# Kernel tuning notes

Hardware: AMD Instinct MI355X
Metric: run time of the kernel (lower is better)

The kernel has to match this reference:

```python
import jax, jax.numpy as jnp
import numpy as np

SEP_ID = 102  # bert-base [SEP]


def setup_inputs() -> dict:
    key = jax.random.key(0)
    B, S, H, M = 64, 512, 768, 21
    k1, k2, k3, k4 = jax.random.split(key, 4)
    hidden = jax.random.normal(k1, (B, S, H), dtype=jnp.float32)  # tf1 last_hidden_state
    ids = jax.random.randint(k2, (B, S), 1000, 30000)
    sep_pos = jnp.arange(24, 24 * (M + 1), 24)  # 21 sep positions < 512
    ids = ids.at[:, sep_pos].set(SEP_ID)
    W = jax.random.normal(k3, (H, H), dtype=jnp.float32) * 0.02  # nn.Linear weight [out,in]
    b = jnp.zeros((H,), dtype=jnp.float32)
    v = jax.random.normal(k4, (H,), dtype=jnp.float32) * 0.02    # linear_value [H,1] squeezed
    return {"hidden": hidden, "input_ids": ids, "W": W, "b": b, "v": v,
            "max_sent_count": M}


def _segment_attention_pool(hidden, input_ids, W, b, v, M):
    B, S, H = hidden.shape
    sep = input_ids == SEP_ID                                 # [B,S] bool
    csum = jnp.cumsum(sep.astype(jnp.int32), axis=1)
    seg = csum - sep.astype(jnp.int32)                        # seps strictly before t
    nsep = csum[:, -1]                                        # sentences per row
    pos = jnp.arange(S)
    # sentence k = tokens strictly between sep k-1 and sep k, excluding CLS (pos 0)
    valid = (~sep) & (pos[None, :] >= 1) & (seg < nsep[:, None]) & (seg < M)

    # attention scores: tanh(x @ W.T + b) @ v
    scores = jnp.einsum('bsh,h->bs', jnp.tanh(jnp.einsum('bsh,kh->bsk', hidden, W) + b), v)

    NS = B * M + 1                                            # +1 dummy segment for invalid tokens
    fid = jnp.where(valid, jnp.arange(B)[:, None] * M + seg, B * M).reshape(-1)
    sflat = jnp.where(valid, scores, -jnp.inf).reshape(-1)

    # per-segment stable softmax
    m = jax.ops.segment_max(sflat, fid, num_segments=NS)
    m = jnp.where(jnp.isfinite(m), m, 0.0)                    # empty segments
    e = jnp.where(valid.reshape(-1), jnp.exp(sflat - m[fid]), 0.0)
    denom = jax.ops.segment_sum(e, fid, num_segments=NS)
    w = e / jnp.where(denom[fid] > 0, denom[fid], 1.0)

    sent = jax.ops.segment_sum(w[:, None] * hidden.reshape(-1, H), fid,
                               num_segments=NS)[:B * M].reshape(B, M, H)
    # rows with zero sentences fall back to the CLS embedding (original behavior)
    sent = sent.at[:, 0, :].set(jnp.where((nsep == 0)[:, None], hidden[:, 0, :], sent[:, 0, :]))
    return sent


def reference(hidden, input_ids, W, b, v, max_sent_count):
    return _segment_attention_pool(hidden, input_ids, W, b, v, max_sent_count)
```

## Files before the change

### kernel.cpp

```cpp
#include <hip/hip_runtime.h>


#define SEP_ID 102
#define Bn 64
#define Sn 512
#define Hn 768
#define Mn 21
#define BS (Bn * Sn)

typedef __attribute__((ext_vector_type(8))) short bf16x8;
typedef __attribute__((ext_vector_type(8))) unsigned short u16x8;
typedef __attribute__((ext_vector_type(4))) float f32x4;

__device__ inline unsigned short f2bf(float x) {
  unsigned int u = __builtin_bit_cast(unsigned int, x);
  u += 0x7fffu + ((u >> 16) & 1u);
  return (unsigned short)(u >> 16);
}

__device__ inline u16x8 cvt8v(f32x4 a, f32x4 b) {
  u16x8 r;
  r[0] = f2bf(a[0]); r[1] = f2bf(a[1]); r[2] = f2bf(a[2]); r[3] = f2bf(a[3]);
  r[4] = f2bf(b[0]); r[5] = f2bf(b[1]); r[6] = f2bf(b[2]); r[7] = f2bf(b[3]);
  return r;
}

__device__ inline float tanh_fast(float x) {
  float e = __builtin_amdgcn_exp2f(x * 2.885390081777927f);
  return 1.f - 2.f * __builtin_amdgcn_rcpf(e + 1.f);
}

__global__ void convw_kernel(const float* __restrict__ W, unsigned short* __restrict__ WBp) {
  int c = blockIdx.x * 256 + threadIdx.x;
  int nt = c / 1536;
  int r  = c % 1536;
  int ks = r >> 6;
  int ln = r & 63;
  int col = nt * 16 + (ln & 15);
  int k0  = ks * 32 + (ln >> 4) * 8;
  const f32x4* src = reinterpret_cast<const f32x4*>(&W[col * Hn + k0]);
  f32x4 a = src[0];
  f32x4 b = src[1];
  *reinterpret_cast<u16x8*>(&WBp[(size_t)c * 8]) = cvt8v(a, b);
}

__global__ void segscan_kernel(const int* __restrict__ ids,
                               unsigned char* __restrict__ segv,
                               int* __restrict__ nsep) {
  int b = blockIdx.x;
  int s = threadIdx.x;
  __shared__ int cs[Sn];
  int sep = (ids[b * Sn + s] == SEP_ID) ? 1 : 0;
  cs[s] = sep;
  __syncthreads();
  for (int off = 1; off < Sn; off <<= 1) {
    int add = (s >= off) ? cs[s - off] : 0;
    __syncthreads();
    cs[s] += add;
    __syncthreads();
  }
  int csum = cs[s];
  int nb = cs[Sn - 1];
  int seg = csum - sep;
  bool valid = (!sep) && (s >= 1) && (seg < nb) && (seg < Mn);
  segv[b * Sn + s] = valid ? (unsigned char)seg : (unsigned char)0xFF;
  if (s == 0) nsep[b] = nb;
}

__global__ __launch_bounds__(1024, 4) void score_gemm_kernel(
    const float* __restrict__ hid, const unsigned short* __restrict__ WBp,
    const float* __restrict__ bbias, const float* __restrict__ vvec,
    float* __restrict__ scores) {
  __shared__ __align__(16) unsigned short As[64 * 768];
  __shared__ float scpart[16][64];

  const int t = threadIdx.x;
  const size_t rowBase = (size_t)blockIdx.x * 64;
  const int wid = t >> 6, lane = t & 63;
  const int l15 = lane & 15, l4 = lane >> 4;
  const int colBase = wid * 48;

  {
    const int srow = t >> 4;
    const int scloc = t & 15;
    const f32x4* hsrc = reinterpret_cast<const f32x4*>(
        &hid[(rowBase + srow) * Hn + scloc * 8]);
    unsigned short* const arow = &As[srow * Hn];
    const int swz = srow & 7;
    f32x4 p[6][2];
#pragma unroll
    for (int cc = 0; cc < 6; ++cc) {
      p[cc][0] = __builtin_nontemporal_load(hsrc + cc * 32);
      p[cc][1] = __builtin_nontemporal_load(hsrc + cc * 32 + 1);
    }
#pragma unroll
    for (int cc = 0; cc < 6; ++cc)
      *reinterpret_cast<u16x8*>(arow + ((cc * 16 + scloc) ^ swz) * 8) =
          cvt8v(p[cc][0], p[cc][1]);
  }
  __syncthreads();

  const unsigned short* const afrow = &As[l15 * Hn];
  const int aswz = l15 & 7;
  const unsigned short* bp0 = &WBp[((size_t)(wid * 3 + 0) * 24 * 64 + lane) * 8];
  const unsigned short* bp1 = &WBp[((size_t)(wid * 3 + 1) * 24 * 64 + lane) * 8];
  const unsigned short* bp2 = &WBp[((size_t)(wid * 3 + 2) * 24 * 64 + lane) * 8];

  f32x4 acc[4][3];
#pragma unroll
  for (int mi = 0; mi < 4; ++mi)
#pragma unroll
    for (int ni = 0; ni < 3; ++ni) acc[mi][ni] = (f32x4){0.f, 0.f, 0.f, 0.f};

  bf16x8 br[4][3];
#pragma unroll
  for (int s = 0; s < 3; ++s) {
    br[s][0] = *reinterpret_cast<const bf16x8*>(bp0 + s * 512);
    br[s][1] = *reinterpret_cast<const bf16x8*>(bp1 + s * 512);
    br[s][2] = *reinterpret_cast<const bf16x8*>(bp2 + s * 512);
  }

#pragma unroll
  for (int kk = 0; kk < 24; ++kk) {
    bf16x8 af[4];
#pragma unroll
    for (int mi = 0; mi < 4; ++mi)
      af[mi] = *reinterpret_cast<const bf16x8*>(
          &afrow[mi * 16 * Hn + (((kk * 4 + l4) ^ aswz)) * 8]);
    if (kk + 3 < 24) {
      const int sl = (kk + 3) & 3;
      br[sl][0] = *reinterpret_cast<const bf16x8*>(bp0 + (kk + 3) * 512);
      br[sl][1] = *reinterpret_cast<const bf16x8*>(bp1 + (kk + 3) * 512);
      br[sl][2] = *reinterpret_cast<const bf16x8*>(bp2 + (kk + 3) * 512);
    }
    const int cu = kk & 3;
    __builtin_amdgcn_s_setprio(1);
#pragma unroll
    for (int mi = 0; mi < 4; ++mi)
#pragma unroll
      for (int ni = 0; ni < 3; ++ni)
        acc[mi][ni] = __builtin_amdgcn_mfma_f32_16x16x32_bf16(
            af[mi], br[cu][ni], acc[mi][ni], 0, 0, 0);
    __builtin_amdgcn_s_setprio(0);
  }

  float sc[4][4];
#pragma unroll
  for (int mi = 0; mi < 4; ++mi)
#pragma unroll
    for (int r = 0; r < 4; ++r) sc[mi][r] = 0.f;
#pragma unroll
  for (int ni = 0; ni < 3; ++ni) {
    int col = colBase + ni * 16 + l15;
    float vv = vvec[col];
    float bb = bbias[col];
#pragma unroll
    for (int mi = 0; mi < 4; ++mi)
#pragma unroll
      for (int r = 0; r < 4; ++r)
        sc[mi][r] += tanh_fast(acc[mi][ni][r] + bb) * vv;
  }
#pragma unroll
  for (int off = 1; off < 16; off <<= 1)
#pragma unroll
    for (int mi = 0; mi < 4; ++mi)
#pragma unroll
      for (int r = 0; r < 4; ++r)
        sc[mi][r] += __shfl_xor(sc[mi][r], off, 64);
  if (l15 == 0) {
#pragma unroll
    for (int mi = 0; mi < 4; ++mi)
#pragma unroll
      for (int r = 0; r < 4; ++r)
        scpart[wid][mi * 16 + l4 * 4 + r] = sc[mi][r];
  }
  __syncthreads();
  if (t < 64) {
    float s = 0.f;
#pragma unroll
    for (int w = 0; w < 16; ++w) s += scpart[w][t];
    scores[rowBase + t] = s;
  }
}

__global__ __launch_bounds__(256) void pool_kernel(
    const float* __restrict__ hid, const float* __restrict__ scores,
    const unsigned char* __restrict__ segv, const int* __restrict__ nsep,
    float* __restrict__ out) {
  int bm = blockIdx.x;
  int b = bm / Mn, m = bm % Mn;
  int t = threadIdx.x;
  __shared__ float wLds[Sn];
  __shared__ float red[256];
  __shared__ int ired[256];
  const float NEG = -1e30f;

  int base = b * Sn;
  unsigned char mg = (unsigned char)m;
  unsigned char g0 = segv[base + t], g1 = segv[base + 256 + t];
  bool v0 = (g0 == mg), v1 = (g1 == mg);
  float s0 = v0 ? scores[base + t] : NEG;
  float s1 = v1 ? scores[base + 256 + t] : NEG;

  red[t] = fmaxf(s0, s1);
  __syncthreads();
  for (int o = 128; o > 0; o >>= 1) {
    if (t < o) red[t] = fmaxf(red[t], red[t + o]);
    __syncthreads();
  }
  float gmax = red[0];
  __syncthreads();

  size_t obase = (size_t)bm * Hn;
  if (gmax <= -0.5e30f) {
    int nb = nsep[b];
    float a0 = 0.f, a1 = 0.f, a2 = 0.f;
    if (m == 0 && nb == 0) {
      const float* hp = hid + (size_t)base * Hn;
      a0 = hp[t]; a1 = hp[t + 256]; a2 = hp[t + 512];
    }
    out[obase + t] = a0; out[obase + 256 + t] = a1; out[obase + 512 + t] = a2;
    return;
  }

  float e0 = v0 ? expf(s0 - gmax) : 0.f;
  float e1 = v1 ? expf(s1 - gmax) : 0.f;
  red[t] = e0 + e1;
  __syncthreads();
  for (int o = 128; o > 0; o >>= 1) {
    if (t < o) red[t] += red[t + o];
    __syncthreads();
  }
  float inv = 1.f / red[0];
  __syncthreads();
  wLds[t] = e0 * inv;
  wLds[256 + t] = e1 * inv;

  ired[t] = min(v0 ? t : 0x7fffffff, v1 ? (256 + t) : 0x7fffffff);
  __syncthreads();
  for (int o = 128; o > 0; o >>= 1) {
    if (t < o) ired[t] = min(ired[t], ired[t + o]);
    __syncthreads();
  }
  int start = ired[0];
  __syncthreads();
  ired[t] = max(v0 ? t : -1, v1 ? (256 + t) : -1);
  __syncthreads();
  for (int o = 128; o > 0; o >>= 1) {
    if (t < o) ired[t] = max(ired[t], ired[t + o]);
    __syncthreads();
  }
  int end = ired[0];
  __syncthreads();

  float a0 = 0.f, a1 = 0.f, a2 = 0.f;
  for (int s = start; s <= end; ++s) {
    float w = wLds[s];
    if (w != 0.f) {
      const float* hp = hid + (size_t)(base + s) * Hn;
      a0 += w * hp[t];
      a1 += w * hp[t + 256];
      a2 += w * hp[t + 512];
    }
  }
  out[obase + t] = a0;
  out[obase + 256 + t] = a1;
  out[obase + 512 + t] = a2;
}

extern "C" void kernel_launch(void* const* d_in, const int* in_sizes, int n_in,
                              void* d_out, int out_size, void* d_ws, size_t ws_size,
                              hipStream_t stream) {
  const float* hidden = (const float*)d_in[0];
  const int* ids      = (const int*)d_in[1];
  const float* W      = (const float*)d_in[2];
  const float* bbias  = (const float*)d_in[3];
  const float* vvec   = (const float*)d_in[4];

  char* ws = (char*)d_ws;
  unsigned short* WBp  = (unsigned short*)(ws);
  float* scores        = (float*)(ws + 1179648);
  unsigned char* segv  = (unsigned char*)(ws + 1310720);
  int* nsep            = (int*)(ws + 1343488);

  convw_kernel<<<288, 256, 0, stream>>>(W, WBp);
  segscan_kernel<<<Bn, Sn, 0, stream>>>(ids, segv, nsep);
  score_gemm_kernel<<<BS / 64, 1024, 0, stream>>>(hidden, WBp, bbias, vvec, scores);
  pool_kernel<<<Bn * Mn, 256, 0, stream>>>(hidden, scores, segv, nsep, (float*)d_out);
}
```

Baseline: 91.25 us.

## Double-buffer A and B fragments with sched barriers in MFMA loop

Replaces the 3-deep register prefetch of B fragments with explicit ping-pong double buffering of both the LDS A fragments and global B fragments, one k-step ahead. A sched_barrier pins the next-step loads ahead of the current MFMA block so their latency overlaps the matrix ops. The hidden-state loads also switch from nontemporal to regular loads. The B prefetch distance drops from three steps to one, which may expose global-load latency.

```diff
diff --git a/kernel.cpp b/kernel.cpp
--- a/kernel.cpp
+++ b/kernel.cpp
@@ -90,8 +90,8 @@
     f32x4 p[6][2];
 #pragma unroll
     for (int cc = 0; cc < 6; ++cc) {
-      p[cc][0] = __builtin_nontemporal_load(hsrc + cc * 32);
-      p[cc][1] = __builtin_nontemporal_load(hsrc + cc * 32 + 1);
+      p[cc][0] = hsrc[cc * 32];
+      p[cc][1] = hsrc[cc * 32 + 1];
     }
 #pragma unroll
     for (int cc = 0; cc < 6; ++cc)
@@ -112,37 +112,43 @@
 #pragma unroll
     for (int ni = 0; ni < 3; ++ni) acc[mi][ni] = (f32x4){0.f, 0.f, 0.f, 0.f};
 
-  bf16x8 br[4][3];
-#pragma unroll
-  for (int s = 0; s < 3; ++s) {
-    br[s][0] = *reinterpret_cast<const bf16x8*>(bp0 + s * 512);
-    br[s][1] = *reinterpret_cast<const bf16x8*>(bp1 + s * 512);
-    br[s][2] = *reinterpret_cast<const bf16x8*>(bp2 + s * 512);
-  }
-
-#pragma unroll
-  for (int kk = 0; kk < 24; ++kk) {
-    bf16x8 af[4];
-#pragma unroll
-    for (int mi = 0; mi < 4; ++mi)
-      af[mi] = *reinterpret_cast<const bf16x8*>(
-          &afrow[mi * 16 * Hn + (((kk * 4 + l4) ^ aswz)) * 8]);
-    if (kk + 3 < 24) {
-      const int sl = (kk + 3) & 3;
-      br[sl][0] = *reinterpret_cast<const bf16x8*>(bp0 + (kk + 3) * 512);
-      br[sl][1] = *reinterpret_cast<const bf16x8*>(bp1 + (kk + 3) * 512);
-      br[sl][2] = *reinterpret_cast<const bf16x8*>(bp2 + (kk + 3) * 512);
-    }
-    const int cu = kk & 3;
-    __builtin_amdgcn_s_setprio(1);
-#pragma unroll
-    for (int mi = 0; mi < 4; ++mi)
-#pragma unroll
-      for (int ni = 0; ni < 3; ++ni)
-        acc[mi][ni] = __builtin_amdgcn_mfma_f32_16x16x32_bf16(
-            af[mi], br[cu][ni], acc[mi][ni], 0, 0, 0);
-    __builtin_amdgcn_s_setprio(0);
-  }
+  bf16x8 afA[4], afB[4], brA[3], brB[3];
+#pragma unroll
+  for (int mi = 0; mi < 4; ++mi)
+    afA[mi] = *reinterpret_cast<const bf16x8*>(
+        &afrow[mi * 16 * Hn + ((l4 ^ aswz)) * 8]);
+  brA[0] = *reinterpret_cast<const bf16x8*>(bp0);
+  brA[1] = *reinterpret_cast<const bf16x8*>(bp1);
+  brA[2] = *reinterpret_cast<const bf16x8*>(bp2);
+
+#define STEP(kk_, afc, afn, brc, brn)                                       \
+  {                                                                         \
+    if ((kk_) < 23) {                                                       \
+      _Pragma("unroll")                                                     \
+      for (int mi = 0; mi < 4; ++mi)                                        \
+        afn[mi] = *reinterpret_cast<const bf16x8*>(                         \
+            &afrow[mi * 16 * Hn + ((((kk_) + 1) * 4 + l4) ^ aswz) * 8]);    \
+      brn[0] = *reinterpret_cast<const bf16x8*>(bp0 + ((kk_) + 1) * 512);   \
+      brn[1] = *reinterpret_cast<const bf16x8*>(bp1 + ((kk_) + 1) * 512);   \
+      brn[2] = *reinterpret_cast<const bf16x8*>(bp2 + ((kk_) + 1) * 512);   \
+    }                                                                       \
+    __builtin_amdgcn_sched_barrier(0);                                      \
+    __builtin_amdgcn_s_setprio(1);                                          \
+    _Pragma("unroll")                                                       \
+    for (int mi = 0; mi < 4; ++mi)                                          \
+      _Pragma("unroll")                                                     \
+      for (int ni = 0; ni < 3; ++ni)                                        \
+        acc[mi][ni] = __builtin_amdgcn_mfma_f32_16x16x32_bf16(              \
+            afc[mi], brc[ni], acc[mi][ni], 0, 0, 0);                        \
+    __builtin_amdgcn_s_setprio(0);                                          \
+  }
+
+#pragma unroll
+  for (int k2 = 0; k2 < 12; ++k2) {
+    STEP(k2 * 2,     afA, afB, brA, brB)
+    STEP(k2 * 2 + 1, afB, afA, brB, brA)
+  }
+#undef STEP
 
   float sc[4][4];
 #pragma unroll
```

Result: faster. 77.58 us (-15.0%).

## Retile score GEMM to 32-row blocks with 8 waves covering 96 columns each

Applied to the files above, without the earlier changes.

The score GEMM now uses 32-row tiles with 512 threads, and each wave covers 6 column tiles instead of 3, for twice as many blocks in the grid. It also drops the explicit 3-deep register prefetch of W fragments and the s_setprio hints, loading B fragments inline each k-step. Hidden loads switch from nontemporal to normal loads. The smaller LDS footprint is meant to raise occupancy and parallelism. The trade-off is that each W fragment is reused across fewer rows, so W traffic doubles, and global-load latency is now less hidden.

```diff
diff --git a/kernel.cpp b/kernel.cpp
--- a/kernel.cpp
+++ b/kernel.cpp
@@ -39,9 +39,7 @@
   int col = nt * 16 + (ln & 15);
   int k0  = ks * 32 + (ln >> 4) * 8;
   const f32x4* src = reinterpret_cast<const f32x4*>(&W[col * Hn + k0]);
-  f32x4 a = src[0];
-  f32x4 b = src[1];
-  *reinterpret_cast<u16x8*>(&WBp[(size_t)c * 8]) = cvt8v(a, b);
+  *reinterpret_cast<u16x8*>(&WBp[(size_t)c * 8]) = cvt8v(src[0], src[1]);
 }
 
 __global__ void segscan_kernel(const int* __restrict__ ids,
@@ -67,18 +65,18 @@
   if (s == 0) nsep[b] = nb;
 }
 
-__global__ __launch_bounds__(1024, 4) void score_gemm_kernel(
+__global__ __launch_bounds__(512, 4) void score_gemm_kernel(
     const float* __restrict__ hid, const unsigned short* __restrict__ WBp,
     const float* __restrict__ bbias, const float* __restrict__ vvec,
     float* __restrict__ scores) {
-  __shared__ __align__(16) unsigned short As[64 * 768];
-  __shared__ float scpart[16][64];
+  __shared__ __align__(16) unsigned short As[32 * 768];
+  __shared__ float scpart[8][32];
 
   const int t = threadIdx.x;
-  const size_t rowBase = (size_t)blockIdx.x * 64;
+  const size_t rowBase = (size_t)blockIdx.x * 32;
   const int wid = t >> 6, lane = t & 63;
   const int l15 = lane & 15, l4 = lane >> 4;
-  const int colBase = wid * 48;
+  const int colBase = wid * 96;
 
   {
     const int srow = t >> 4;
@@ -90,8 +88,8 @@
     f32x4 p[6][2];
 #pragma unroll
     for (int cc = 0; cc < 6; ++cc) {
-      p[cc][0] = __builtin_nontemporal_load(hsrc + cc * 32);
-      p[cc][1] = __builtin_nontemporal_load(hsrc + cc * 32 + 1);
+      p[cc][0] = hsrc[cc * 32];
+      p[cc][1] = hsrc[cc * 32 + 1];
     }
 #pragma unroll
     for (int cc = 0; cc < 6; ++cc)
@@ -102,60 +100,48 @@
 
   const unsigned short* const afrow = &As[l15 * Hn];
   const int aswz = l15 & 7;
-  const unsigned short* bp0 = &WBp[((size_t)(wid * 3 + 0) * 24 * 64 + lane) * 8];
-  const unsigned short* bp1 = &WBp[((size_t)(wid * 3 + 1) * 24 * 64 + lane) * 8];
-  const unsigned short* bp2 = &WBp[((size_t)(wid * 3 + 2) * 24 * 64 + lane) * 8];
-
-  f32x4 acc[4][3];
-#pragma unroll
-  for (int mi = 0; mi < 4; ++mi)
-#pragma unroll
-    for (int ni = 0; ni < 3; ++ni) acc[mi][ni] = (f32x4){0.f, 0.f, 0.f, 0.f};
-
-  bf16x8 br[4][3];
-#pragma unroll
-  for (int s = 0; s < 3; ++s) {
-    br[s][0] = *reinterpret_cast<const bf16x8*>(bp0 + s * 512);
-    br[s][1] = *reinterpret_cast<const bf16x8*>(bp1 + s * 512);
-    br[s][2] = *reinterpret_cast<const bf16x8*>(bp2 + s * 512);
-  }
+  const unsigned short* bp[6];
+#pragma unroll
+  for (int ni = 0; ni < 6; ++ni)
+    bp[ni] = &WBp[((size_t)(wid * 6 + ni) * 24 * 64 + lane) * 8];
+
+  f32x4 acc[2][6];
+#pragma unroll
+  for (int mi = 0; mi < 2; ++mi)
+#pragma unroll
+    for (int ni = 0; ni < 6; ++ni) acc[mi][ni] = (f32x4){0.f, 0.f, 0.f, 0.f};
 
 #pragma unroll
   for (int kk = 0; kk < 24; ++kk) {
-    bf16x8 af[4];
-#pragma unroll
-    for (int mi = 0; mi < 4; ++mi)
+    bf16x8 af[2];
+#pragma unroll
+    for (int mi = 0; mi < 2; ++mi)
       af[mi] = *reinterpret_cast<const bf16x8*>(
           &afrow[mi * 16 * Hn + (((kk * 4 + l4) ^ aswz)) * 8]);
-    if (kk + 3 < 24) {
-      const int sl = (kk + 3) & 3;
-      br[sl][0] = *reinterpret_cast<const bf16x8*>(bp0 + (kk + 3) * 512);
-      br[sl][1] = *reinterpret_cast<const bf16x8*>(bp1 + (kk + 3) * 512);
-      br[sl][2] = *reinterpret_cast<const bf16x8*>(bp2 + (kk + 3) * 512);
-    }
-    const int cu = kk & 3;
-    __builtin_amdgcn_s_setprio(1);
-#pragma unroll
-    for (int mi = 0; mi < 4; ++mi)
-#pragma unroll
-      for (int ni = 0; ni < 3; ++ni)
+    bf16x8 br[6];
+#pragma unroll
+    for (int ni = 0; ni < 6; ++ni)
+      br[ni] = *reinterpret_cast<const bf16x8*>(bp[ni] + kk * 512);
+#pragma unroll
+    for (int mi = 0; mi < 2; ++mi)
+#pragma unroll
+      for (int ni = 0; ni < 6; ++ni)
         acc[mi][ni] = __builtin_amdgcn_mfma_f32_16x16x32_bf16(
-            af[mi], br[cu][ni], acc[mi][ni], 0, 0, 0);
-    __builtin_amdgcn_s_setprio(0);
-  }
-
-  float sc[4][4];
-#pragma unroll
-  for (int mi = 0; mi < 4; ++mi)
+            af[mi], br[ni], acc[mi][ni], 0, 0, 0);
+  }
+
+  float sc[2][4];
+#pragma unroll
+  for (int mi = 0; mi < 2; ++mi)
 #pragma unroll
     for (int r = 0; r < 4; ++r) sc[mi][r] = 0.f;
 #pragma unroll
-  for (int ni = 0; ni < 3; ++ni) {
+  for (int ni = 0; ni < 6; ++ni) {
     int col = colBase + ni * 16 + l15;
     float vv = vvec[col];
     float bb = bbias[col];
 #pragma unroll
-    for (int mi = 0; mi < 4; ++mi)
+    for (int mi = 0; mi < 2; ++mi)
 #pragma unroll
       for (int r = 0; r < 4; ++r)
         sc[mi][r] += tanh_fast(acc[mi][ni][r] + bb) * vv;
@@ -163,22 +149,22 @@
 #pragma unroll
   for (int off = 1; off < 16; off <<= 1)
 #pragma unroll
-    for (int mi = 0; mi < 4; ++mi)
+    for (int mi = 0; mi < 2; ++mi)
 #pragma unroll
       for (int r = 0; r < 4; ++r)
         sc[mi][r] += __shfl_xor(sc[mi][r], off, 64);
   if (l15 == 0) {
 #pragma unroll
-    for (int mi = 0; mi < 4; ++mi)
+    for (int mi = 0; mi < 2; ++mi)
 #pragma unroll
       for (int r = 0; r < 4; ++r)
         scpart[wid][mi * 16 + l4 * 4 + r] = sc[mi][r];
   }
   __syncthreads();
-  if (t < 64) {
+  if (t < 32) {
     float s = 0.f;
 #pragma unroll
-    for (int w = 0; w < 16; ++w) s += scpart[w][t];
+    for (int w = 0; w < 8; ++w) s += scpart[w][t];
     scores[rowBase + t] = s;
   }
 }
@@ -285,6 +271,6 @@
 
   convw_kernel<<<288, 256, 0, stream>>>(W, WBp);
   segscan_kernel<<<Bn, Sn, 0, stream>>>(ids, segv, nsep);
-  score_gemm_kernel<<<BS / 64, 1024, 0, stream>>>(hidden, WBp, bbias, vvec, scores);
+  score_gemm_kernel<<<BS / 32, 512, 0, stream>>>(hidden, WBp, bbias, vvec, scores);
   pool_kernel<<<Bn * Mn, 256, 0, stream>>>(hidden, scores, segv, nsep, (float*)d_out);
 }
```

After: 86.56 us. 1.05x faster.
